# Kernel optimization log

Measured on AMD Instinct MI355X. Metric: run time of the kernel, lower is better.

The kernel has to match this reference:

```python
import jax, jax.numpy as jnp
import numpy as np

# Llama-2-7B-like GQA attention, prefill over packed equal-length sequences
H = 4096      # hidden_size
NH = 32       # num_attention_heads
NKV = 8       # num_key_value_heads
HD = H // NH  # head_dim = 128
B = 4         # number of packed sequences
S = 1024      # seq_len per sequence
T = B * S     # total packed tokens
BASE = 10000.0  # rope_theta


def setup_inputs() -> dict:
    key = jax.random.key(0)
    ks = jax.random.split(key, 5)
    x = jax.random.normal(ks[0], (T, H), jnp.float32)
    positions = jnp.tile(jnp.arange(S, dtype=jnp.int32), B)  # per-seq positions
    kv_cache = jnp.zeros((1,), jnp.float32)  # placeholder (prefill: kv from current tokens)
    init = 0.02
    wq = jax.random.normal(ks[1], (NH * HD, H), jnp.float32) * init
    wk = jax.random.normal(ks[2], (NKV * HD, H), jnp.float32) * init
    wv = jax.random.normal(ks[3], (NKV * HD, H), jnp.float32) * init
    wo = jax.random.normal(ks[4], (H, NH * HD), jnp.float32) * init
    return {"x": x, "positions": positions, "kv_cache": kv_cache,
            "wq": wq, "wk": wk, "wv": wv, "wo": wo, "seq_len": S}


def _rope(xh, cos_b, sin_b):
    # xh: [T, Hh, D]; cos_b/sin_b: [T, 1, D] (freqs repeat-interleaved by 2)
    half = xh.shape[-1] // 2
    x_rot = jnp.concatenate([-xh[..., half:], xh[..., :half]], axis=-1)
    return xh * cos_b + x_rot * sin_b


def reference(x, positions, kv_cache, wq, wk, wv, wo, seq_len):
    Tn = x.shape[0]
    q = (x @ wq.T).reshape(Tn, NH, HD)
    k = (x @ wk.T).reshape(Tn, NKV, HD)
    v = (x @ wv.T).reshape(Tn, NKV, HD)
    # GQA: repeat_interleave kv heads
    rep = NH // NKV
    k = jnp.repeat(k, rep, axis=1)
    v = jnp.repeat(v, rep, axis=1)
    # RoPE tables (faithful to _precompute_freqs/_rotary_embeddings)
    inv_freq = 1.0 / (BASE ** (jnp.arange(0, HD, 2, dtype=jnp.float32) / HD))
    t = jnp.arange(seq_len, dtype=jnp.float32)
    freqs = t[:, None] * inv_freq[None, :]            # [S, D/2]
    cos, sin = jnp.cos(freqs), jnp.sin(freqs)
    pos = jnp.clip(positions.astype(jnp.int32), 0, seq_len - 1)
    cos_b = jnp.repeat(cos[pos], 2, axis=-1)[:, None, :]  # [T,1,D]
    sin_b = jnp.repeat(sin[pos], 2, axis=-1)[:, None, :]
    q = _rope(q, cos_b, sin_b)
    k = _rope(k, cos_b, sin_b)
    # Paged attention (prefill): causal attention within each packed sequence
    Bn = Tn // seq_len
    qb = q.reshape(Bn, seq_len, NH, HD)
    kb = k.reshape(Bn, seq_len, NH, HD)
    vb = v.reshape(Bn, seq_len, NH, HD)
    scores = jnp.einsum('bqhd,bkhd->bhqk', qb, kb) * (HD ** -0.5)
    causal = jnp.tril(jnp.ones((seq_len, seq_len), bool))
    scores = jnp.where(causal[None, None], scores, -jnp.inf)
    probs = jax.nn.softmax(scores, axis=-1)
    out = jnp.einsum('bhqk,bkhd->bqhd', probs, vb).reshape(Tn, NH * HD)
    return out @ wo.T
```

## Files before the change

kernel.cpp:

```cpp
#include <hip/hip_runtime.h>
#include <hip/hip_bf16.h>
#include <math.h>

#define T_TOK 4096
#define HID   4096
#define NHQ   32
#define NKVH  8
#define HDIM  128
#define SEQ   1024
#define NBATCH 4

typedef __attribute__((ext_vector_type(8))) short bf16x8;
typedef __attribute__((ext_vector_type(4))) float f32x4;

__device__ __forceinline__ unsigned short f2bf(float f) {
  union { float f; unsigned int u; } x; x.f = f;
  unsigned int r = x.u + 0x7FFFu + ((x.u >> 16) & 1u);
  return (unsigned short)(r >> 16);
}

#define GLOAD_LDS16(gp, lp)                                                        \
  __builtin_amdgcn_global_load_lds(                                                \
      (__attribute__((address_space(1))) void*)(unsigned long long)(const void*)(gp), \
      (__attribute__((address_space(3))) void*)(unsigned long long)(const void*)(lp), \
      16, 0, 0)

__global__ __launch_bounds__(256) void cast_all_k(const float* __restrict__ x,
                                                  const float* __restrict__ wq,
                                                  const float* __restrict__ wk,
                                                  const float* __restrict__ wv,
                                                  const float* __restrict__ wo,
                                                  unsigned short* __restrict__ xb,
                                                  unsigned short* __restrict__ wqkv,
                                                  unsigned short* __restrict__ wob) {
  int i = blockIdx.x * 256 + threadIdx.x;
  const float* src; unsigned short* dst; int off;
  if (i < 4194304)       { src = x;  dst = xb;   off = i; }
  else if (i < 8388608)  { src = wq; dst = wqkv; off = i - 4194304; }
  else if (i < 9437184)  { src = wk; dst = wqkv + 16777216; off = i - 8388608; }
  else if (i < 10485760) { src = wv; dst = wqkv + 20971520; off = i - 9437184; }
  else                   { src = wo; dst = wob;  off = i - 10485760; }
  float4 f = ((const float4*)src)[off];
  ushort4 o;
  o.x = f2bf(f.x); o.y = f2bf(f.y); o.z = f2bf(f.z); o.w = f2bf(f.w);
  ((ushort4*)dst)[off] = o;
}

template<bool FUSED>
__global__ __launch_bounds__(512, 2) void gemm8(const unsigned short* __restrict__ A,
                                                const unsigned short* __restrict__ B,
                                                float* __restrict__ C,
                                                const int* __restrict__ pos,
                                                unsigned short* __restrict__ qr,
                                                unsigned short* __restrict__ kr,
                                                unsigned short* __restrict__ vbuf,
                                                int N, int K) {
  __shared__ unsigned short As[3][16384];
  __shared__ unsigned short Bs[3][8192];
  const int tid  = threadIdx.x;
  const int lane = tid & 63;
  const int wave = tid >> 6;
  const int m16  = lane & 15;
  const int quad = lane >> 4;
  const int wm   = wave >> 1;
  const int wn   = wave & 1;

  const int gx = gridDim.x;
  const int nwg = gx * gridDim.y;
  const int orig = blockIdx.y * gx + blockIdx.x;
  const int swz = (orig & 7) * (nwg >> 3) + (orig >> 3);
  const long rowBase = (long)(swz / gx) * 256;
  const long colBase = (long)(swz % gx) * 128;

  const long Kl = K;
  const int sck = ((tid & 7) ^ (((tid >> 5) & 1) << 1)) * 8;
  const unsigned short* sA = A + (rowBase + (tid >> 3)) * Kl + sck;
  const unsigned short* sB = B + (colBase + (tid >> 3)) * Kl + sck;
  const int dofs = wave * 512;

#define STG_A01(sl_, ko_) { GLOAD_LDS16(sA + (ko_),           &As[sl_][dofs]);          \
                            GLOAD_LDS16(sA + (ko_) + 64*Kl,   &As[sl_][4096 + dofs]); }
#define STG_A23(sl_, ko_) { GLOAD_LDS16(sA + (ko_) + 128*Kl,  &As[sl_][8192 + dofs]);   \
                            GLOAD_LDS16(sA + (ko_) + 192*Kl,  &As[sl_][12288 + dofs]); }
#define STG_B01(sl_, ko_) { GLOAD_LDS16(sB + (ko_),           &Bs[sl_][dofs]);          \
                            GLOAD_LDS16(sB + (ko_) + 64*Kl,   &Bs[sl_][4096 + dofs]); }

#define RDA(dv_, mfr_, ks_) {                                                     \
    int row_ = wm * 64 + (mfr_) * 16 + m16;                                       \
    dv_ = *(const bf16x8*)(Aq + row_ * 64 + ((((ks_)*4 + quad)*8) ^ ((row_ & 4) << 2))); }
#define RDB(dv_, nf_, ks_) {                                                      \
    int row_ = wn * 32 + ((nf_) & 1) * 16 + ((nf_) >> 1) * 64 + m16;              \
    dv_ = *(const bf16x8*)(Bq + row_ * 64 + ((((ks_)*4 + quad)*8) ^ ((row_ & 4) << 2))); }

  f32x4 acc[4][4] = {};
  const int nt = K >> 6;

  STG_A01(0, 0); STG_A23(0, 0); STG_B01(0, 0);
  STG_A01(1, 64); STG_A23(1, 64); STG_B01(1, 64);
  asm volatile("s_waitcnt vmcnt(6)" ::: "memory");
  __builtin_amdgcn_s_barrier();

  int sl = 0;
  for (int t = 0; t < nt; ++t) {
    const unsigned short* Aq = &As[sl][0];
    const unsigned short* Bq = &Bs[sl][0];
    const int s2 = sl >= 1 ? sl - 1 : 2;
    const bool doStage = (t + 2) < nt;
    const long ko = (long)(t + 2) * 64;

    bf16x8 af[2][2], bf[4][2];
#pragma unroll
    for (int mf = 0; mf < 2; ++mf)
#pragma unroll
      for (int ks = 0; ks < 2; ++ks) RDA(af[mf][ks], mf, ks);
#pragma unroll
    for (int nf = 0; nf < 4; ++nf)
#pragma unroll
      for (int ks = 0; ks < 2; ++ks) RDB(bf[nf][ks], nf, ks);
    if (doStage) STG_A01(s2, ko);
    asm volatile("s_waitcnt lgkmcnt(8)" ::: "memory");
    __builtin_amdgcn_s_barrier();
    __builtin_amdgcn_s_setprio(1);
#pragma unroll
    for (int mf = 0; mf < 2; ++mf)
#pragma unroll
      for (int nf = 0; nf < 4; ++nf)
#pragma unroll
        for (int ks = 0; ks < 2; ++ks)
          acc[mf][nf] = __builtin_amdgcn_mfma_f32_16x16x32_bf16(af[mf][ks], bf[nf][ks], acc[mf][nf], 0, 0, 0);
    __builtin_amdgcn_s_setprio(0);
    __builtin_amdgcn_s_barrier();

#pragma unroll
    for (int mf = 0; mf < 2; ++mf)
#pragma unroll
      for (int ks = 0; ks < 2; ++ks) RDA(af[mf][ks], 2 + mf, ks);
    if (doStage) { STG_A23(s2, ko); STG_B01(s2, ko); }
    if (doStage)         asm volatile("s_waitcnt vmcnt(6)" ::: "memory");
    else if (t + 1 < nt) asm volatile("s_waitcnt vmcnt(0)" ::: "memory");
    __builtin_amdgcn_s_barrier();
    __builtin_amdgcn_s_setprio(1);
#pragma unroll
    for (int mf = 0; mf < 2; ++mf)
#pragma unroll
      for (int nf = 0; nf < 4; ++nf)
#pragma unroll
        for (int ks = 0; ks < 2; ++ks)
          acc[2 + mf][nf] = __builtin_amdgcn_mfma_f32_16x16x32_bf16(af[mf][ks], bf[nf][ks], acc[2 + mf][nf], 0, 0, 0);
    __builtin_amdgcn_s_setprio(0);
    __builtin_amdgcn_s_barrier();

    sl = sl == 2 ? 0 : sl + 1;
  }

  if (!FUSED) {
#pragma unroll
    for (int mf = 0; mf < 4; ++mf)
#pragma unroll
      for (int nf = 0; nf < 4; ++nf) {
        long c = colBase + wn * 32 + (nf & 1) * 16 + (nf >> 1) * 64 + m16;
#pragma unroll
        for (int reg = 0; reg < 4; ++reg) {
          long row = rowBase + wm * 64 + mf * 16 + quad * 4 + reg;
          C[row * N + c] = acc[mf][nf][reg];
        }
      }
    return;
  }

  const int n0 = (int)colBase;
  unsigned short* dst;
  int rstride, colofs;
  bool dorope;
  if (n0 < 4096)       { dst = qr;   rstride = NHQ * HDIM;  colofs = n0;        dorope = true; }
  else if (n0 < 5120)  { dst = kr;   rstride = NKVH * HDIM; colofs = n0 - 4096; dorope = true; }
  else                 { dst = vbuf; rstride = NKVH * HDIM; colofs = n0 - 5120; dorope = false; }
  const float c0 = -13.287712379549449f / 64.0f;
  float fA[2], fB[2];
#pragma unroll
  for (int e = 0; e < 2; ++e) {
    int d = wn * 32 + e * 16 + m16;
    fA[e] = exp2f(c0 * (float)(d >> 1));
    fB[e] = exp2f(c0 * (float)((d >> 1) + 32));
  }
#pragma unroll
  for (int mf = 0; mf < 4; ++mf) {
#pragma unroll
    for (int reg = 0; reg < 4; ++reg) {
      int grow = (int)rowBase + wm * 64 + mf * 16 + quad * 4 + reg;
      unsigned short* drow = dst + (long)grow * rstride + colofs;
      if (dorope) {
        int p = pos[grow];
        p = p < 0 ? 0 : (p > SEQ - 1 ? SEQ - 1 : p);
        float pf = (float)p;
#pragma unroll
        for (int e = 0; e < 2; ++e) {
          int d = wn * 32 + e * 16 + m16;
          float lo = acc[mf][e][reg], hi = acc[mf][e + 2][reg];
          float s1, cc1, s2, cc2;
          __sincosf(pf * fA[e], &s1, &cc1);
          __sincosf(pf * fB[e], &s2, &cc2);
          drow[d]      = f2bf(lo * cc1 - hi * s1);
          drow[d + 64] = f2bf(hi * cc2 + lo * s2);
        }
      } else {
#pragma unroll
        for (int e = 0; e < 2; ++e) {
          int d = wn * 32 + e * 16 + m16;
          drow[d]      = f2bf(acc[mf][e][reg]);
          drow[d + 64] = f2bf(acc[mf][e + 2][reg]);
        }
      }
    }
  }
}

#define ATT_SCALE_L2 0.12754227022f
__global__ __launch_bounds__(256) void attn_k(const unsigned short* __restrict__ Qp,
                                              const unsigned short* __restrict__ Kp,
                                              const unsigned short* __restrict__ Vp,
                                              unsigned short* __restrict__ Op) {
  const int pr = blockIdx.x, h = blockIdx.y, b = blockIdx.z;
  const int kvh = h >> 2;
  const int tid = threadIdx.x, wave = tid >> 6, lane = tid & 63;
  const int m16 = lane & 15, quad = lane >> 4;

  __shared__ unsigned short Ks[64][128];
  __shared__ unsigned short Vt[128][64];
  __shared__ unsigned short Ps[4][32][64];

  for (int pass = 0; pass < 2; ++pass) {
    const int qt = pass ? pr : (7 - pr);
    const int qbase = qt * 128;
    const int wq_lo = qbase + wave * 32;

    bf16x8 qa[2][4];
#pragma unroll
    for (int i = 0; i < 2; ++i) {
      const unsigned short* qrow =
          Qp + (long)(b * SEQ + wq_lo + i * 16 + m16) * (NHQ * HDIM) + h * HDIM;
#pragma unroll
      for (int kk = 0; kk < 4; ++kk)
        qa[i][kk] = *(const bf16x8*)(qrow + kk * 32 + quad * 8);
    }

    f32x4 o[2][8] = {};
    float mrow[2][4], lrow[2][4];
#pragma unroll
    for (int i = 0; i < 2; ++i)
#pragma unroll
      for (int r = 0; r < 4; ++r) { mrow[i][r] = -1e30f; lrow[i][r] = 0.f; }

    const int nkt = qt * 2 + 2;
    for (int kt = 0; kt < nkt; ++kt) {
      __syncthreads();
      const unsigned short* Kbase =
          Kp + (long)(b * SEQ + kt * 64) * (NKVH * HDIM) + kvh * HDIM;
      const unsigned short* Vbase =
          Vp + (long)(b * SEQ + kt * 64) * (NKVH * HDIM) + kvh * HDIM;
#pragma unroll
      for (int it = 0; it < 4; ++it) {
        int c = it * 256 + tid;
        int row = c >> 4, psg = c & 15;
        int sg = (psg & 8) | ((psg & 7) ^ (row & 7));
        GLOAD_LDS16(Kbase + row * (NKVH * HDIM) + sg * 8,
                    ((unsigned short*)Ks) + (it * 256 + wave * 64) * 8);
      }
#pragma unroll
      for (int it = 0; it < 4; ++it) {
        int seg = it * 4 + wave;
        uint4 dv = *(const uint4*)(Vbase + lane * (NKVH * HDIM) + seg * 8);
        const unsigned short* pv = (const unsigned short*)&dv;
#pragma unroll
        for (int e = 0; e < 8; ++e) {
          int d = seg * 8 + e;
          Vt[d][((((lane >> 3) + d) & 7) * 8) + (lane & 7)] = pv[e];
        }
      }
      __syncthreads();

      const bool active = (kt * 64) <= (wq_lo + 31);
      if (active) {
        f32x4 s4[2][4] = {};
#pragma unroll
        for (int kk = 0; kk < 4; ++kk) {
          bf16x8 kbf[4];
#pragma unroll
          for (int j = 0; j < 4; ++j) {
            int row = j * 16 + m16;
            int cl = kk * 4 + quad;
            int ps = (cl & 8) | ((cl & 7) ^ (row & 7));
            kbf[j] = *(const bf16x8*)(&Ks[row][ps * 8]);
          }
#pragma unroll
          for (int i = 0; i < 2; ++i)
#pragma unroll
            for (int j = 0; j < 4; ++j)
              s4[i][j] = __builtin_amdgcn_mfma_f32_16x16x32_bf16(qa[i][kk], kbf[j], s4[i][j], 0, 0, 0);
        }
        const bool full = (kt * 64 + 63) <= wq_lo;
#pragma unroll
        for (int i = 0; i < 2; ++i) {
#pragma unroll
          for (int r = 0; r < 4; ++r) {
            const int qrow = i * 16 + quad * 4 + r;
            const int qi = qbase + wave * 32 + qrow;
            float v[4];
#pragma unroll
            for (int j = 0; j < 4; ++j) {
              v[j] = s4[i][j][r] * ATT_SCALE_L2;
              if (!full && (kt * 64 + j * 16 + m16 > qi)) v[j] = -1e30f;
            }
            float mx = fmaxf(fmaxf(v[0], v[1]), fmaxf(v[2], v[3]));
            mx = fmaxf(mx, __shfl_xor(mx, 1));
            mx = fmaxf(mx, __shfl_xor(mx, 2));
            mx = fmaxf(mx, __shfl_xor(mx, 4));
            mx = fmaxf(mx, __shfl_xor(mx, 8));
            float mold = mrow[i][r];
            float mnew = fmaxf(mold, mx);
            float alpha = exp2f(mold - mnew);
            float rs = 0.f;
#pragma unroll
            for (int j = 0; j < 4; ++j) {
              float pj = exp2f(v[j] - mnew);
              rs += pj;
              int col = j * 16 + m16;
              Ps[wave][qrow][((((col >> 3) + qrow) & 7) * 8) + (col & 7)] = f2bf(pj);
            }
            rs += __shfl_xor(rs, 1); rs += __shfl_xor(rs, 2);
            rs += __shfl_xor(rs, 4); rs += __shfl_xor(rs, 8);
            lrow[i][r] = lrow[i][r] * alpha + rs;
            mrow[i][r] = mnew;
#pragma unroll
            for (int n = 0; n < 8; ++n) o[i][n][r] *= alpha;
          }
        }
#pragma unroll
        for (int kk = 0; kk < 2; ++kk) {
          bf16x8 pa[2], vb[8];
#pragma unroll
          for (int i = 0; i < 2; ++i) {
            int row = i * 16 + m16;
            pa[i] = *(const bf16x8*)(&Ps[wave][row][(((kk * 4 + quad) + row) & 7) * 8]);
          }
#pragma unroll
          for (int n = 0; n < 8; ++n) {
            int row = n * 16 + m16;
            vb[n] = *(const bf16x8*)(&Vt[row][(((kk * 4 + quad) + row) & 7) * 8]);
          }
#pragma unroll
          for (int i = 0; i < 2; ++i)
#pragma unroll
            for (int n = 0; n < 8; ++n)
              o[i][n] = __builtin_amdgcn_mfma_f32_16x16x32_bf16(pa[i], vb[n], o[i][n], 0, 0, 0);
        }
      }
    }
#pragma unroll
    for (int i = 0; i < 2; ++i) {
#pragma unroll
      for (int r = 0; r < 4; ++r) {
        float inv = 1.0f / lrow[i][r];
        unsigned short* orow =
            Op + (long)(b * SEQ + wq_lo + i * 16 + quad * 4 + r) * (NHQ * HDIM) + h * HDIM;
#pragma unroll
        for (int n = 0; n < 8; ++n)
          orow[n * 16 + m16] = f2bf(o[i][n][r] * inv);
      }
    }
  }
}

extern "C" void kernel_launch(void* const* d_in, const int* in_sizes, int n_in,
                              void* d_out, int out_size, void* d_ws, size_t ws_size,
                              hipStream_t stream) {
  (void)in_sizes; (void)n_in; (void)out_size; (void)ws_size;
  const float* x  = (const float*)d_in[0];
  const int* pos  = (const int*)d_in[1];
  const float* wq = (const float*)d_in[3];
  const float* wk = (const float*)d_in[4];
  const float* wv = (const float*)d_in[5];
  const float* wo = (const float*)d_in[6];
  float* out = (float*)d_out;

  char* ws = (char*)d_ws;
  unsigned short* xb    = (unsigned short*)(ws);
  unsigned short* wqkv  = (unsigned short*)(ws + (32ll << 20));
  unsigned short* wob   = (unsigned short*)(ws + (80ll << 20));
  unsigned short* qr    = (unsigned short*)(ws + (112ll << 20));
  unsigned short* kr    = (unsigned short*)(ws + (144ll << 20));
  unsigned short* vb_   = (unsigned short*)(ws + (152ll << 20));
  unsigned short* ao    = (unsigned short*)(ws + (160ll << 20));

  cast_all_k<<<57344, 256, 0, stream>>>(x, wq, wk, wv, wo, xb, wqkv, wob);
  gemm8<true><<<dim3(48, 16), 512, 0, stream>>>(xb, wqkv, nullptr, pos, qr, kr, vb_, 6144, 4096);
  attn_k<<<dim3(4, 32, 4), 256, 0, stream>>>(qr, kr, vb_, ao);
  gemm8<false><<<dim3(32, 16), 512, 0, stream>>>(ao, wob, out, nullptr, nullptr, nullptr, nullptr, 4096, 4096);
}
```

Measured before the change: 810.7 us.

## Restructure GEMM main loop with split A/B LDS buffering and unrolled phases

Replaces the three-slot shared A/B ring with a two-slot A buffer and a four-slot B buffer. The K loop is unrolled by four, with the loop count hardcoded to 64 K-tiles (K=4096), and each step is split into two MFMA phases over B column halves. The LDS swizzle changes to a full 3-bit XOR, and LDS read offsets are precomputed. The goal is to overlap global-to-LDS staging with MFMA work and cut bank conflicts. In exchange, the loop only works for K=4096, and refilling the A buffer while it may still be in use needs careful barrier ordering.

Result: faster. 754.0 us (-7.0%).

```diff
diff --git a/kernel.cpp b/kernel.cpp
--- a/kernel.cpp
+++ b/kernel.cpp
@@ -55,8 +55,8 @@
                                                 unsigned short* __restrict__ kr,
                                                 unsigned short* __restrict__ vbuf,
                                                 int N, int K) {
-  __shared__ unsigned short As[3][16384];
-  __shared__ unsigned short Bs[3][8192];
+  __shared__ unsigned short AL[2][16384];
+  __shared__ unsigned short BL[4][8192];
   const int tid  = threadIdx.x;
   const int lane = tid & 63;
   const int wave = tid >> 6;
@@ -72,85 +72,85 @@
   const long rowBase = (long)(swz / gx) * 256;
   const long colBase = (long)(swz % gx) * 128;
 
+  int aoff[2], boff[2];
+#pragma unroll
+  for (int ks = 0; ks < 2; ++ks) {
+    int sx = ((ks * 4 + quad) ^ (m16 & 7)) * 8;
+    aoff[ks] = (wm * 64 + m16) * 64 + sx;
+    boff[ks] = (wn * 32 + m16) * 64 + sx;
+  }
+
   const long Kl = K;
-  const int sck = ((tid & 7) ^ (((tid >> 5) & 1) << 1)) * 8;
-  const unsigned short* sA = A + (rowBase + (tid >> 3)) * Kl + sck;
-  const unsigned short* sB = B + (colBase + (tid >> 3)) * Kl + sck;
+  const int sck = ((tid & 7) ^ ((tid >> 3) & 7)) * 8;
+  const unsigned short* gA = A + (rowBase + (tid >> 3)) * Kl + sck;
+  const unsigned short* gB = B + (colBase + (tid >> 3)) * Kl + sck;
   const int dofs = wave * 512;
 
-#define STG_A01(sl_, ko_) { GLOAD_LDS16(sA + (ko_),           &As[sl_][dofs]);          \
-                            GLOAD_LDS16(sA + (ko_) + 64*Kl,   &As[sl_][4096 + dofs]); }
-#define STG_A23(sl_, ko_) { GLOAD_LDS16(sA + (ko_) + 128*Kl,  &As[sl_][8192 + dofs]);   \
-                            GLOAD_LDS16(sA + (ko_) + 192*Kl,  &As[sl_][12288 + dofs]); }
-#define STG_B01(sl_, ko_) { GLOAD_LDS16(sB + (ko_),           &Bs[sl_][dofs]);          \
-                            GLOAD_LDS16(sB + (ko_) + 64*Kl,   &Bs[sl_][4096 + dofs]); }
-
-#define RDA(dv_, mfr_, ks_) {                                                     \
-    int row_ = wm * 64 + (mfr_) * 16 + m16;                                       \
-    dv_ = *(const bf16x8*)(Aq + row_ * 64 + ((((ks_)*4 + quad)*8) ^ ((row_ & 4) << 2))); }
-#define RDB(dv_, nf_, ks_) {                                                      \
-    int row_ = wn * 32 + ((nf_) & 1) * 16 + ((nf_) >> 1) * 64 + m16;              \
-    dv_ = *(const bf16x8*)(Bq + row_ * 64 + ((((ks_)*4 + quad)*8) ^ ((row_ & 4) << 2))); }
+#define STG_B(slot_, ko_) { GLOAD_LDS16(gB + (ko_),            &BL[slot_][dofs]);         \
+                            GLOAD_LDS16(gB + (ko_) + 64 * Kl,  &BL[slot_][4096 + dofs]); }
+#define STG_A(slot_, ko_) { GLOAD_LDS16(gA + (ko_),            &AL[slot_][dofs]);         \
+                            GLOAD_LDS16(gA + (ko_) + 64 * Kl,  &AL[slot_][4096 + dofs]);  \
+                            GLOAD_LDS16(gA + (ko_) + 128 * Kl, &AL[slot_][8192 + dofs]);  \
+                            GLOAD_LDS16(gA + (ko_) + 192 * Kl, &AL[slot_][12288 + dofs]); }
 
   f32x4 acc[4][4] = {};
-  const int nt = K >> 6;
-
-  STG_A01(0, 0); STG_A23(0, 0); STG_B01(0, 0);
-  STG_A01(1, 64); STG_A23(1, 64); STG_B01(1, 64);
+
+  STG_B(0, 0); STG_A(0, 0); STG_B(1, 64); STG_A(1, 64);
   asm volatile("s_waitcnt vmcnt(6)" ::: "memory");
   __builtin_amdgcn_s_barrier();
 
-  int sl = 0;
-  for (int t = 0; t < nt; ++t) {
-    const unsigned short* Aq = &As[sl][0];
-    const unsigned short* Bq = &Bs[sl][0];
-    const int s2 = sl >= 1 ? sl - 1 : 2;
-    const bool doStage = (t + 2) < nt;
-    const long ko = (long)(t + 2) * 64;
-
-    bf16x8 af[2][2], bf[4][2];
-#pragma unroll
-    for (int mf = 0; mf < 2; ++mf)
-#pragma unroll
-      for (int ks = 0; ks < 2; ++ks) RDA(af[mf][ks], mf, ks);
-#pragma unroll
-    for (int nf = 0; nf < 4; ++nf)
-#pragma unroll
-      for (int ks = 0; ks < 2; ++ks) RDB(bf[nf][ks], nf, ks);
-    if (doStage) STG_A01(s2, ko);
-    asm volatile("s_waitcnt lgkmcnt(8)" ::: "memory");
-    __builtin_amdgcn_s_barrier();
-    __builtin_amdgcn_s_setprio(1);
-#pragma unroll
-    for (int mf = 0; mf < 2; ++mf)
-#pragma unroll
-      for (int nf = 0; nf < 4; ++nf)
+  for (int it = 0; it < 16; ++it) {
+#pragma unroll
+    for (int u = 0; u < 4; ++u) {
+      const int X = it * 4 + u;
+      const int kn = ((X + 2) & 63) << 6;
+      bf16x8 af[4][2], bf01[2][2], bf23[2][2];
+
+#pragma unroll
+      for (int mf = 0; mf < 4; ++mf)
 #pragma unroll
         for (int ks = 0; ks < 2; ++ks)
-          acc[mf][nf] = __builtin_amdgcn_mfma_f32_16x16x32_bf16(af[mf][ks], bf[nf][ks], acc[mf][nf], 0, 0, 0);
-    __builtin_amdgcn_s_setprio(0);
-    __builtin_amdgcn_s_barrier();
-
-#pragma unroll
-    for (int mf = 0; mf < 2; ++mf)
-#pragma unroll
-      for (int ks = 0; ks < 2; ++ks) RDA(af[mf][ks], 2 + mf, ks);
-    if (doStage) { STG_A23(s2, ko); STG_B01(s2, ko); }
-    if (doStage)         asm volatile("s_waitcnt vmcnt(6)" ::: "memory");
-    else if (t + 1 < nt) asm volatile("s_waitcnt vmcnt(0)" ::: "memory");
-    __builtin_amdgcn_s_barrier();
-    __builtin_amdgcn_s_setprio(1);
-#pragma unroll
-    for (int mf = 0; mf < 2; ++mf)
-#pragma unroll
-      for (int nf = 0; nf < 4; ++nf)
+          af[mf][ks] = *(const bf16x8*)(&AL[u & 1][aoff[ks] + mf * 1024]);
+#pragma unroll
+      for (int nf = 0; nf < 2; ++nf)
 #pragma unroll
         for (int ks = 0; ks < 2; ++ks)
-          acc[2 + mf][nf] = __builtin_amdgcn_mfma_f32_16x16x32_bf16(af[mf][ks], bf[nf][ks], acc[2 + mf][nf], 0, 0, 0);
-    __builtin_amdgcn_s_setprio(0);
-    __builtin_amdgcn_s_barrier();
-
-    sl = sl == 2 ? 0 : sl + 1;
+          bf01[nf][ks] = *(const bf16x8*)(&BL[u][boff[ks] + nf * 1024]);
+      STG_B((u + 2) & 3, kn);
+      asm volatile("s_waitcnt lgkmcnt(8)" ::: "memory");
+      __builtin_amdgcn_s_barrier();
+      asm volatile("s_waitcnt lgkmcnt(0)" ::: "memory");
+      __builtin_amdgcn_s_setprio(1);
+#pragma unroll
+      for (int mf = 0; mf < 4; ++mf)
+#pragma unroll
+        for (int nf = 0; nf < 2; ++nf)
+#pragma unroll
+          for (int ks = 0; ks < 2; ++ks)
+            acc[mf][nf] = __builtin_amdgcn_mfma_f32_16x16x32_bf16(af[mf][ks], bf01[nf][ks], acc[mf][nf], 0, 0, 0);
+      __builtin_amdgcn_s_setprio(0);
+      __builtin_amdgcn_s_barrier();
+
+#pragma unroll
+      for (int nf = 0; nf < 2; ++nf)
+#pragma unroll
+        for (int ks = 0; ks < 2; ++ks)
+          bf23[nf][ks] = *(const bf16x8*)(&BL[u][boff[ks] + nf * 1024 + 4096]);
+      STG_A(u & 1, kn);
+      __builtin_amdgcn_s_barrier();
+      asm volatile("s_waitcnt lgkmcnt(0)" ::: "memory");
+      __builtin_amdgcn_s_setprio(1);
+#pragma unroll
+      for (int mf = 0; mf < 4; ++mf)
+#pragma unroll
+        for (int nf = 0; nf < 2; ++nf)
+#pragma unroll
+          for (int ks = 0; ks < 2; ++ks)
+            acc[mf][nf + 2] = __builtin_amdgcn_mfma_f32_16x16x32_bf16(af[mf][ks], bf23[nf][ks], acc[mf][nf + 2], 0, 0, 0);
+      __builtin_amdgcn_s_setprio(0);
+      asm volatile("s_waitcnt vmcnt(6)" ::: "memory");
+      __builtin_amdgcn_s_barrier();
+    }
   }
 
   if (!FUSED) {
```
